# Kernel optimization log

Hardware: AMD Instinct MI355X
Metric: run time of the kernel (lower is better)

Reference implementation:

```python
import math
import jax, jax.numpy as jnp
import numpy as np

B, L, D, H = 8, 4096, 512, 8
FACTOR = 1


def setup_inputs() -> dict:
    key = jax.random.key(0)
    ks = jax.random.split(key, 8)
    scale = 0.02
    return {
        "queries": jax.random.normal(ks[0], (B, L, D), dtype=jnp.float32),
        "keys": jax.random.normal(ks[1], (B, L, D), dtype=jnp.float32),
        "values": jax.random.normal(ks[2], (B, L, D), dtype=jnp.float32),
        "Wq": jax.random.normal(ks[3], (D, D), dtype=jnp.float32) * scale,
        "bq": jnp.zeros((D,), dtype=jnp.float32),
        "Wk": jax.random.normal(ks[4], (D, D), dtype=jnp.float32) * scale,
        "bk": jnp.zeros((D,), dtype=jnp.float32),
        "Wv": jax.random.normal(ks[5], (D, D), dtype=jnp.float32) * scale,
        "bv": jnp.zeros((D,), dtype=jnp.float32),
        "Wo": jax.random.normal(ks[6], (D, D), dtype=jnp.float32) * scale,
        "bo": jnp.zeros((D,), dtype=jnp.float32),
    }


def reference(queries, keys, values, Wq, bq, Wk, bk, Wv, bv, Wo, bo):
    b, l, d = queries.shape
    h = H
    e = d // h
    # Projections (torch Linear math; weight stored as [in, out] here)
    q = (queries @ Wq + bq).reshape(b, l, h, e)
    k = (keys @ Wk + bk).reshape(b, l, h, e)
    v = (values @ Wv + bv).reshape(b, l, h, e)
    # [B, H, E, L]
    qp = q.transpose(0, 2, 3, 1)
    kp = k.transpose(0, 2, 3, 1)
    vp = v.transpose(0, 2, 3, 1)
    # FFT cross-correlation over the time axis
    qf = jnp.fft.rfft(qp, axis=-1)
    kf = jnp.fft.rfft(kp, axis=-1)
    corr = jnp.fft.irfft(qf * jnp.conj(kf), n=l, axis=-1)  # [B,H,E,L]
    # time_delay_agg_training
    top_k = int(FACTOR * math.log(l))
    mean_value = corr.mean(axis=(1, 2))  # [B, L] (mean over head then channel)
    _, index = jax.lax.top_k(mean_value.mean(axis=0), top_k)  # [K] shared delays
    weights = mean_value[:, index]  # [B, K]
    tmp_corr = jax.nn.softmax(weights, axis=-1)  # [B, K]
    # roll(values, -delay) along time == gather at (t + delay) mod L
    idx = (jnp.arange(l)[None, :] + index[:, None]) % l  # [K, L]
    gathered = jnp.take(vp, idx, axis=-1)  # [B, H, E, K, L]
    agg = jnp.einsum("bhekl,bk->bhel", gathered, tmp_corr)  # weighted MAC over delays
    out = agg.transpose(0, 3, 1, 2).reshape(b, l, h * e)  # [B, L, D]
    return out @ Wo + bo
```

## Files before the change

kernel.cpp:

```cpp
#include <hip/hip_runtime.h>
#include <math.h>

#define LSEQ 4096
#define DMODEL 512
#define BB 8
#define TOPK 8
#define ML (BB * LSEQ)
#define FFT_CH 2
#define NGRP (DMODEL / FFT_CH)
#define PPH 2052

typedef unsigned short u16;
typedef unsigned int u32;
typedef float f32x4 __attribute__((ext_vector_type(4)));
typedef short s16x8 __attribute__((ext_vector_type(8)));
typedef u16 u16x8 __attribute__((ext_vector_type(8)));

__device__ __forceinline__ u16 rne_bf16(float f) {
    u32 u = __float_as_uint(f);
    return (u16)((u + 0x7FFF + ((u >> 16) & 1)) >> 16);
}

__device__ __forceinline__ uint4 cvt8(const float4 f0, const float4 f1) {
    float fs[8] = {f0.x, f0.y, f0.z, f0.w, f1.x, f1.y, f1.z, f1.w};
    u32 h[4];
#pragma unroll
    for (int p = 0; p < 4; ++p) {
        u32 u0 = __float_as_uint(fs[2 * p]);
        u32 u1 = __float_as_uint(fs[2 * p + 1]);
        u32 h0 = u0 + 0x7FFF + ((u0 >> 16) & 1);
        u32 h1 = u1 + 0x7FFF + ((u1 >> 16) & 1);
        h[p] = __builtin_amdgcn_perm(h1, h0, 0x07060302u);
    }
    return make_uint4(h[0], h[1], h[2], h[3]);
}

#if defined(__has_builtin)
#if __has_builtin(__builtin_amdgcn_global_load_lds)
#define HAVE_GLL 1
#endif
#endif

__device__ __forceinline__ void gload_lds16(const u16* g, u16* lbase, int lane) {
#ifdef HAVE_GLL
    __builtin_amdgcn_global_load_lds((const __attribute__((address_space(1))) void*)g,
                                     (__attribute__((address_space(3))) void*)lbase, 16, 0, 0);
#else
    *(uint4*)(lbase + lane * 8) = *(const uint4*)g;
#endif
}

__device__ __forceinline__ void fft16(float (&zr)[16], float (&zi)[16]) {
    const float C1 = 0.92387953251128674f, S1 = 0.38268343236508978f, R2 = 0.70710678118654752f;
#define BF0(i, j) { float ar=zr[i],ai=zi[i],br=zr[j],bi=zi[j]; zr[i]=ar+br; zi[i]=ai+bi; zr[j]=ar-br; zi[j]=ai-bi; }
#define BFW(i, j, wr, wi) { float ar=zr[i],ai=zi[i],br=zr[j],bi=zi[j]; zr[i]=ar+br; zi[i]=ai+bi; float dr=ar-br, di=ai-bi; zr[j]=dr*(wr)-di*(wi); zi[j]=dr*(wi)+di*(wr); }
#define BFI(i, j) { float ar=zr[i],ai=zi[i],br=zr[j],bi=zi[j]; zr[i]=ar+br; zi[i]=ai+bi; float dr=ar-br, di=ai-bi; zr[j]=di; zi[j]=-dr; }
    BF0(0, 8); BFW(1, 9, C1, -S1); BFW(2, 10, R2, -R2); BFW(3, 11, S1, -C1);
    BFI(4, 12); BFW(5, 13, -S1, -C1); BFW(6, 14, -R2, -R2); BFW(7, 15, -C1, -S1);
    BF0(0, 4); BFW(1, 5, R2, -R2); BFI(2, 6); BFW(3, 7, -R2, -R2);
    BF0(8, 12); BFW(9, 13, R2, -R2); BFI(10, 14); BFW(11, 15, -R2, -R2);
    BF0(0, 2); BFI(1, 3); BF0(4, 6); BFI(5, 7);
    BF0(8, 10); BFI(9, 11); BF0(12, 14); BFI(13, 15);
    BF0(0, 1); BF0(2, 3); BF0(4, 5); BF0(6, 7);
    BF0(8, 9); BF0(10, 11); BF0(12, 13); BF0(14, 15);
#undef BF0
#undef BFW
#undef BFI
}

template <bool WRITEBACK>
__device__ __forceinline__ void fft4096_r16_core(float* __restrict__ lre, float* __restrict__ lim, int t,
                                                 float (&ozr)[16], float (&ozi)[16]) {
    constexpr int REV16[16] = {0, 8, 4, 12, 2, 10, 6, 14, 1, 9, 5, 13, 3, 11, 7, 15};
    float zr[16], zi[16];
#pragma unroll
    for (int gg = 0; gg < 16; ++gg) {
        int n = 256 * gg + t;
        int p = n ^ ((gg & 3) << 2) ^ ((gg & 1) << 4);
        zr[gg] = lre[p]; zi[gg] = lim[p];
    }
    fft16(zr, zi);
    {
        const int n1 = t >> 4;
        float w1i, w1r;
        __sincosf(-0.0245436926061702596f * (float)n1, &w1i, &w1r);
        float wr = 1.f, wi = 0.f;
#pragma unroll
        for (int k0 = 0; k0 < 16; ++k0) {
            float vr = zr[REV16[k0]], vi = zi[REV16[k0]];
            if (k0) {
                float nr = wr * w1r - wi * w1i;
                wi = wr * w1i + wi * w1r;
                wr = nr;
                float tr = vr * wr - vi * wi;
                vi = vr * wi + vi * wr;
                vr = tr;
            }
            int n = 256 * k0 + t;
            int p = n ^ ((k0 & 3) << 2) ^ ((k0 & 1) << 4);
            lre[p] = vr; lim[p] = vi;
        }
    }
    __syncthreads();
    {
        const int k0 = t >> 4, n2 = t & 15;
        const int x0 = ((k0 & 3) << 2) | ((k0 & 1) << 4);
#pragma unroll
        for (int gg = 0; gg < 16; ++gg) {
            int n = 256 * k0 + 16 * gg + n2;
            zr[gg] = lre[n ^ x0]; zi[gg] = lim[n ^ x0];
        }
        fft16(zr, zi);
        float wbi, wbr, wsi, wsr;
        __sincosf(-0.00153398078788564123f * (float)(n2 * k0), &wbi, &wbr);
        __sincosf(-0.0245436926061702596f * (float)n2, &wsi, &wsr);
        float wr = wbr, wi = wbi;
#pragma unroll
        for (int k1 = 0; k1 < 16; ++k1) {
            float vr = zr[REV16[k1]], vi = zi[REV16[k1]];
            if (k1) {
                float nr = wr * wsr - wi * wsi;
                wi = wr * wsi + wi * wsr;
                wr = nr;
            }
            float tr = vr * wr - vi * wi;
            vi = vr * wi + vi * wr;
            vr = tr;
            int n = 256 * k0 + 16 * k1 + n2;
            lre[n ^ x0] = vr; lim[n ^ x0] = vi;
        }
    }
    __syncthreads();
    {
        const int k0 = t & 15, k1 = t >> 4;
        const int nb4 = 64 * k0 + 4 * k1;
        const int xv = (k0 & 3) | ((k0 & 1) << 2);
#pragma unroll
        for (int i = 0; i < 4; ++i) {
            int p4 = (nb4 + i) ^ xv;
            float4 fr = *(const float4*)&lre[4 * p4];
            float4 fi = *(const float4*)&lim[4 * p4];
            ozr[4 * i + 0] = fr.x; ozr[4 * i + 1] = fr.y; ozr[4 * i + 2] = fr.z; ozr[4 * i + 3] = fr.w;
            ozi[4 * i + 0] = fi.x; ozi[4 * i + 1] = fi.y; ozi[4 * i + 2] = fi.z; ozi[4 * i + 3] = fi.w;
        }
        fft16(ozr, ozi);
        if constexpr (WRITEBACK) {
            __syncthreads();
#pragma unroll
            for (int r = 0; r < 16; ++r) {
                const int k2 = REV16[r];
                lre[t + 256 * k2] = ozr[r];
                lim[t + 256 * k2] = ozi[r];
            }
            __syncthreads();
        }
    }
}

__global__ __launch_bounds__(256) void fft_cross(const u16* __restrict__ Qtb,
                                                 const u16* __restrict__ Ktb,
                                                 float* __restrict__ Ppart) {
    __shared__ float lre[4096];
    __shared__ float lim[4096];
    constexpr int REV16[16] = {0, 8, 4, 12, 2, 10, 6, 14, 1, 9, 5, 13, 3, 11, 7, 15};
    const int t = threadIdx.x;
    const int b = blockIdx.x / NGRP;
    const int g = blockIdx.x % NGRP;

    float2 acc[8];
#pragma unroll
    for (int i = 0; i < 8; ++i) acc[i] = make_float2(0.f, 0.f);
    float accn = 0.f;

    const uint4* q8 = (const uint4*)(Qtb + (size_t)(g * FFT_CH) * ML + (size_t)b * LSEQ);
    const uint4* k8 = (const uint4*)(Ktb + (size_t)(g * FFT_CH) * ML + (size_t)b * LSEQ);

    uint4 pq[2], pk[2];
    pq[0] = q8[t]; pq[1] = q8[t + 256];
    pk[0] = k8[t]; pk[1] = k8[t + 256];

    for (int c = 0; c < FFT_CH; ++c) {
        __syncthreads();
#pragma unroll
        for (int i = 0; i < 2; ++i) {
            const int u = t + 256 * i;
            const uint4 vq = pq[i], vk = pk[i];
#pragma unroll
            for (int hh = 0; hh < 2; ++hh) {
                const int v = 2 * u + hh;
                const int key = (v >> 6) & 15;
                const int p4 = v ^ (key & 3) ^ ((key & 1) << 2);
                const u32 w0 = hh ? vq.z : vq.x;
                const u32 w1 = hh ? vq.w : vq.y;
                float4 fa = make_float4(__uint_as_float(w0 << 16), __uint_as_float(w0 & 0xFFFF0000u),
                                        __uint_as_float(w1 << 16), __uint_as_float(w1 & 0xFFFF0000u));
                *(float4*)&lre[4 * p4] = fa;
                const u32 x0 = hh ? vk.z : vk.x;
                const u32 x1 = hh ? vk.w : vk.y;
                float4 fb = make_float4(__uint_as_float(x0 << 16), __uint_as_float(x0 & 0xFFFF0000u),
                                        __uint_as_float(x1 << 16), __uint_as_float(x1 & 0xFFFF0000u));
                *(float4*)&lim[4 * p4] = fb;
            }
        }
        if (c + 1 < FFT_CH) {
            const uint4* qn = q8 + (size_t)(c + 1) * (ML / 8);
            const uint4* kn = k8 + (size_t)(c + 1) * (ML / 8);
            pq[0] = qn[t]; pq[1] = qn[t + 256];
            pk[0] = kn[t]; pk[1] = kn[t + 256];
        }
        __syncthreads();
        float ozr[16], ozi[16];
        fft4096_r16_core<true>(lre, lim, t, ozr, ozi);
#pragma unroll
        for (int i = 0; i < 8; ++i) {
            const int j = i * 256 + t;
            const int nj = (4096 - j) & 4095;
            const int r = REV16[i];
            float zfr = ozr[r], zfi = ozi[r];
            float znr = lre[nj], zni = lim[nj];
            float qr = 0.5f * (zfr + znr);
            float qi = 0.5f * (zfi - zni);
            float kr = 0.5f * (zfi + zni);
            float ki = -0.5f * (zfr - znr);
            acc[i].x += qr * kr + qi * ki;
            acc[i].y += qi * kr - qr * ki;
        }
        if (t == 0) accn += ozr[1] * ozi[1];
    }
    float2* Pp = (float2*)Ppart + (size_t)blockIdx.x * PPH;
#pragma unroll
    for (int i = 0; i < 8; ++i) Pp[i * 256 + t] = acc[i];
    if (t == 0) Pp[2048] = make_float2(accn, 0.f);
}

template <bool TOUT, bool BIAS>
__device__ __forceinline__ void gemm_bf16_body(const u16* __restrict__ A,
                                               const u16* __restrict__ B,
                                               const float* __restrict__ bias,
                                               u16* __restrict__ Cv, int lin, int tid,
                                               u16* sA, u16* sB) {
    const int t = (lin & 7) * 128 + (lin >> 3);
    const int bm = (t >> 2) * 128;
    const int bn = (t & 3) * 128;
    const int lane = tid & 63, wid = tid >> 6;
    const int wm = wid >> 1, wn = wid & 1;
    const int l15 = lane & 15, kg = lane >> 4;

    const int srow = lane >> 3, sc = lane & 7;

    f32x4 acc[4][4] = {};

    for (int k0 = 0; k0 < 512; k0 += 64) {
        __syncthreads();
#pragma unroll
        for (int i = 0; i < 4; ++i) {
            const int grp = wid * 4 + i;
            const int row = 8 * grp + srow;
            gload_lds16(A + (size_t)(bm + row) * 512 + k0 + ((sc ^ (row & 7)) << 3),
                        sA + grp * 512, lane);
        }
#pragma unroll
        for (int i = 0; i < 4; ++i) {
            const int grp = wid * 4 + i;
            const int row = 8 * grp + srow;
            gload_lds16(B + (size_t)(bn + row) * 512 + k0 + ((sc ^ (row & 7)) << 3),
                        sB + grp * 512, lane);
        }
        __syncthreads();
#pragma unroll
        for (int kk = 0; kk < 2; ++kk) {
            const int cb = kk * 4 + kg;
            s16x8 af[4], bf[4];
#pragma unroll
            for (int mi = 0; mi < 4; ++mi) {
                const int row = wm * 64 + mi * 16 + l15;
                af[mi] = *(const s16x8*)&sA[row * 64 + (((cb ^ (row & 7))) << 3)];
            }
#pragma unroll
            for (int ni = 0; ni < 4; ++ni) {
                const int row = wn * 64 + ni * 16 + l15;
                bf[ni] = *(const s16x8*)&sB[row * 64 + (((cb ^ (row & 7))) << 3)];
            }
#pragma unroll
            for (int ni = 0; ni < 4; ++ni)
#pragma unroll
                for (int mi = 0; mi < 4; ++mi)
                    acc[mi][ni] = __builtin_amdgcn_mfma_f32_16x16x32_bf16(af[mi], bf[ni], acc[mi][ni], 0, 0, 0);
        }
    }
    if constexpr (TOUT) {
#pragma unroll
        for (int ni = 0; ni < 4; ++ni) {
            const int d = bn + wn * 64 + ni * 16 + l15;
#pragma unroll
            for (int mi = 0; mi < 4; ++mi) {
                const int rb = bm + wm * 64 + mi * 16 + (kg << 2);
                ushort4 o;
                o.x = rne_bf16(acc[mi][ni][0]); o.y = rne_bf16(acc[mi][ni][1]);
                o.z = rne_bf16(acc[mi][ni][2]); o.w = rne_bf16(acc[mi][ni][3]);
                *(ushort4*)&Cv[(size_t)d * ML + rb] = o;
            }
        }
    } else {
#pragma unroll
        for (int ni = 0; ni < 4; ++ni) {
            const int col = bn + wn * 64 + ni * 16 + l15;
            const float bvv = BIAS ? bias[col] : 0.0f;
#pragma unroll
            for (int mi = 0; mi < 4; ++mi) {
                const int rb = bm + wm * 64 + mi * 16 + (kg << 2);
#pragma unroll
                for (int r = 0; r < 4; ++r)
                    Cv[(size_t)(rb + r) * 512 + col] = rne_bf16(acc[mi][ni][r] + bvv);
            }
        }
    }
}

__global__ __launch_bounds__(256) void gemm2(const u16* __restrict__ Qb,
                                             const u16* __restrict__ Mh, u16* __restrict__ Qtb,
                                             const u16* __restrict__ Vb,
                                             const u16* __restrict__ Wch, const float* __restrict__ bc,
                                             u16* __restrict__ VOb) {
    __shared__ __align__(16) u16 smem[16384];
    const int g = blockIdx.x;
    const int q = g >> 1, r = g & 1;
    if (r == 0)
        gemm_bf16_body<true, false>(Qb, Mh, nullptr, Qtb, q, threadIdx.x, smem, smem + 8192);
    else
        gemm_bf16_body<false, true>(Vb, Wch, bc, VOb, q, threadIdx.x, smem, smem + 8192);
}

__global__ __launch_bounds__(256) void prep_stream(const float* __restrict__ Wq, const float* __restrict__ Wk,
                                                   const float* __restrict__ Wv, const float* __restrict__ Wo,
                                                   const float* __restrict__ bvec, const float* __restrict__ bo,
                                                   u16* __restrict__ Mh, u16* __restrict__ Wch,
                                                   float* __restrict__ bc,
                                                   const float* __restrict__ keys, u16* __restrict__ Ktb,
                                                   const float* __restrict__ queries, u16* __restrict__ Qb,
                                                   const float* __restrict__ values, u16* __restrict__ Vb) {
    __shared__ __align__(16) char smem[16896];
    const int bx = blockIdx.x;
    const int tid = threadIdx.x;
    if (bx < 128) {
        float (*As)[64] = (float (*)[64])smem;
        float (*Ws)[64] = (float (*)[64])(smem + 4096);
        const bool isM = bx < 64;
        const int id = bx & 63;
        const int bm = (id >> 3) * 64, bn = (id & 7) * 64;
        const int tx = tid & 15, ty = tid >> 4;
        float acc[4][4] = {};
        const int arow = tid >> 2, ak4 = tid & 3;
        const int wrow = tid >> 4, wc4 = tid & 15;
        const float* Abase = isM ? Wq : Wv;
        for (int k0 = 0; k0 < 512; k0 += 16) {
            float4 av = *(const float4*)&Abase[(size_t)(bm + arow) * 512 + k0 + ak4 * 4];
            float4 wv4;
            if (isM) wv4 = *(const float4*)&Wk[(size_t)(bn + arow) * 512 + k0 + ak4 * 4];
            else     wv4 = *(const float4*)&Wo[(size_t)(k0 + wrow) * 512 + bn + wc4 * 4];
            __syncthreads();
            As[ak4 * 4 + 0][arow] = av.x;
            As[ak4 * 4 + 1][arow] = av.y;
            As[ak4 * 4 + 2][arow] = av.z;
            As[ak4 * 4 + 3][arow] = av.w;
            if (isM) {
                Ws[ak4 * 4 + 0][arow] = wv4.x;
                Ws[ak4 * 4 + 1][arow] = wv4.y;
                Ws[ak4 * 4 + 2][arow] = wv4.z;
                Ws[ak4 * 4 + 3][arow] = wv4.w;
            } else {
                *(float4*)&Ws[wrow][wc4 * 4] = wv4;
            }
            __syncthreads();
#pragma unroll
            for (int k = 0; k < 16; ++k) {
                float4 a = *(const float4*)&As[k][ty * 4];
                float4 b = *(const float4*)&Ws[k][tx * 4];
                acc[0][0] += a.x * b.x; acc[0][1] += a.x * b.y; acc[0][2] += a.x * b.z; acc[0][3] += a.x * b.w;
                acc[1][0] += a.y * b.x; acc[1][1] += a.y * b.y; acc[1][2] += a.y * b.z; acc[1][3] += a.y * b.w;
                acc[2][0] += a.z * b.x; acc[2][1] += a.z * b.y; acc[2][2] += a.z * b.z; acc[2][3] += a.z * b.w;
                acc[3][0] += a.w * b.x; acc[3][1] += a.w * b.y; acc[3][2] += a.w * b.z; acc[3][3] += a.w * b.w;
            }
        }
        u16* dh = isM ? Mh : Wch;
#pragma unroll
        for (int i = 0; i < 4; ++i)
#pragma unroll
            for (int j = 0; j < 4; ++j) {
                const int a = bm + ty * 4 + i;
                const int n = bn + tx * 4 + j;
                dh[(size_t)n * 512 + a] = rne_bf16(acc[i][j]);
            }
    } else if (bx < 144) {
        float (*red)[32] = (float (*)[32])smem;
        const int n0 = (bx - 128) * 32;
        const int nl = tid & 31, jg = tid >> 5;
        float partial = 0.f;
        for (int s = 0; s < 64; ++s) {
            int j = jg + 8 * s;
            partial += bvec[j] * Wo[(size_t)j * 512 + n0 + nl];
        }
        red[jg][nl] = partial;
        __syncthreads();
        if (tid < 32) {
            float s2 = 0.f;
            for (int r2 = 0; r2 < 8; ++r2) s2 += red[r2][tid];
            bc[n0 + tid] = s2 + bo[n0 + tid];
        }
    } else if (bx < 144 + 4096) {
        float* Ts = (float*)smem;
        const int tb = bx - 144;
        const int bd = (tb & 7) * 64;
        const int bm = (tb >> 3) * 64;
        const int rr = tid >> 2, c4 = tid & 3;
#pragma unroll
        for (int i = 0; i < 4; ++i) {
            const int c0 = (c4 + 4 * i) * 4;
            float4 v = *(const float4*)&keys[(size_t)(bm + rr) * DMODEL + bd + c0];
            Ts[rr * 65 + c0 + 0] = v.x; Ts[rr * 65 + c0 + 1] = v.y;
            Ts[rr * 65 + c0 + 2] = v.z; Ts[rr * 65 + c0 + 3] = v.w;
        }
        __syncthreads();
        const int dl = tid >> 2, m4 = tid & 3;
#pragma unroll
        for (int i = 0; i < 4; ++i) {
            const int m0 = (m4 + 4 * i) * 4;
            ushort4 o;
            o.x = rne_bf16(Ts[(m0 + 0) * 65 + dl]);
            o.y = rne_bf16(Ts[(m0 + 1) * 65 + dl]);
            o.z = rne_bf16(Ts[(m0 + 2) * 65 + dl]);
            o.w = rne_bf16(Ts[(m0 + 3) * 65 + dl]);
            *(ushort4*)&Ktb[(size_t)(bd + dl) * ML + bm + m0] = o;
        }
    } else {
        const int idx = bx - (144 + 4096);
        const float* src = (idx < 8192) ? queries : values;
        u16* dst = (idx < 8192) ? Qb : Vb;
        const size_t base = (size_t)(idx & 8191) * 2048 + tid * 8;
        float4 f0 = *(const float4*)&src[base];
        float4 f1 = *(const float4*)&src[base + 4];
        *(uint4*)&dst[base] = cvt8(f0, f1);
    }
}

__global__ __launch_bounds__(256) void reduce_ppart(const float2* __restrict__ Pp,
                                                    float2* __restrict__ Pred4) {
    const int j = blockIdx.x * 256 + threadIdx.x;
    const int b = blockIdx.y;
    const int z = blockIdx.z;
    if (j > 2048) return;
    float sr = 0.f, si = 0.f;
    const float2* base = Pp + (size_t)b * NGRP * PPH + j;
    for (int g = z * 64; g < z * 64 + 64; ++g) {
        float2 p = base[(size_t)g * PPH];
        sr += p.x;
        si += p.y;
    }
    Pred4[((size_t)z * BB + b) * PPH + j] = make_float2(sr, si);
}

__global__ __launch_bounds__(256) void ifft_mean(const float2* __restrict__ Pred4,
                                                 float* __restrict__ mv) {
    __shared__ float lre[4096];
    __shared__ float lim[4096];
    constexpr int REV16[16] = {0, 8, 4, 12, 2, 10, 6, 14, 1, 9, 5, 13, 3, 11, 7, 15};
    const int t = threadIdx.x;
    const int b = blockIdx.x;
    for (int j = t; j < 4096; j += 256) {
        const int jj = (j <= 2048) ? j : 4096 - j;
        float sr = 0.f, si = 0.f;
#pragma unroll
        for (int z = 0; z < 4; ++z) {
            float2 p = Pred4[((size_t)z * BB + b) * PPH + jj];
            sr += p.x;
            si += p.y;
        }
        if (j > 2048) si = -si;
        int key = (j >> 8) & 15;
        int ph = j ^ ((key & 3) << 2) ^ ((key & 1) << 4);
        lre[ph] = sr;
        lim[ph] = -si;
    }
    __syncthreads();
    float ozr[16], ozi[16];
    fft4096_r16_core<false>(lre, lim, t, ozr, ozi);
    const float scale = 1.0f / (4096.0f * 512.0f);
#pragma unroll
    for (int i = 0; i < 16; ++i)
        mv[(size_t)b * 4096 + t + 256 * i] = ozr[REV16[i]] * scale;
}

__global__ __launch_bounds__(1024) void topk_softmax(const float* __restrict__ mv,
                                                     int* __restrict__ idxO,
                                                     float* __restrict__ tcO) {
    __shared__ float vals[4096];
    __shared__ float wv[16];
    __shared__ int wix[16];
    __shared__ int sidx[TOPK];
    const int tid = threadIdx.x;
    const int lane = tid & 63, wvid = tid >> 6;
    for (int j = tid; j < 4096; j += 1024) {
        float s = 0.f;
        for (int b = 0; b < BB; ++b) s += mv[(size_t)b * 4096 + j];
        vals[j] = s * 0.125f;
    }
    __syncthreads();
    for (int k = 0; k < TOPK; ++k) {
        float best = -INFINITY;
        int bi = 0x7fffffff;
        for (int j = tid; j < 4096; j += 1024) {
            float v = vals[j];
            if (v > best) { best = v; bi = j; }
        }
#pragma unroll
        for (int off = 32; off > 0; off >>= 1) {
            float ov = __shfl_down(best, off);
            int oi = __shfl_down(bi, off);
            if (ov > best || (ov == best && oi < bi)) { best = ov; bi = oi; }
        }
        if (lane == 0) { wv[wvid] = best; wix[wvid] = bi; }
        __syncthreads();
        if (wvid == 0) {
            best = (lane < 16) ? wv[lane] : -INFINITY;
            bi = (lane < 16) ? wix[lane] : 0x7fffffff;
#pragma unroll
            for (int off = 8; off > 0; off >>= 1) {
                float ov = __shfl_down(best, off);
                int oi = __shfl_down(bi, off);
                if (ov > best || (ov == best && oi < bi)) { best = ov; bi = oi; }
            }
            if (lane == 0) {
                sidx[k] = bi;
                idxO[k] = bi;
                vals[bi] = -INFINITY;
            }
        }
        __syncthreads();
    }
    if (tid < BB) {
        float w[TOPK];
        float m = -INFINITY;
        for (int k = 0; k < TOPK; ++k) {
            w[k] = mv[(size_t)tid * 4096 + sidx[k]];
            m = fmaxf(m, w[k]);
        }
        float s = 0.f;
        for (int k = 0; k < TOPK; ++k) { w[k] = expf(w[k] - m); s += w[k]; }
        float inv = 1.0f / s;
        for (int k = 0; k < TOPK; ++k) tcO[tid * TOPK + k] = w[k] * inv;
    }
}

__global__ __launch_bounds__(256) void gather_out(const u16* __restrict__ VO,
                                                  const int* __restrict__ idx,
                                                  const float* __restrict__ tc,
                                                  float* __restrict__ out) {
    const int e = blockIdx.x * 256 + threadIdx.x;
    const int d8 = e & 63;
    const int l = (e >> 6) & 4095;
    const int b = e >> 18;
    float s[8] = {};
#pragma unroll
    for (int k = 0; k < TOPK; ++k) {
        const int src = (l + idx[k]) & 4095;
        const float w = tc[b * TOPK + k];
        uint4 v = *(const uint4*)&VO[((size_t)(b * 4096 + src)) * 512 + d8 * 8];
        s[0] += w * __uint_as_float(v.x << 16);
        s[1] += w * __uint_as_float(v.x & 0xFFFF0000u);
        s[2] += w * __uint_as_float(v.y << 16);
        s[3] += w * __uint_as_float(v.y & 0xFFFF0000u);
        s[4] += w * __uint_as_float(v.z << 16);
        s[5] += w * __uint_as_float(v.z & 0xFFFF0000u);
        s[6] += w * __uint_as_float(v.w << 16);
        s[7] += w * __uint_as_float(v.w & 0xFFFF0000u);
    }
    const size_t ob = ((size_t)(b * 4096 + l)) * 512 + d8 * 8;
    *(float4*)&out[ob]     = make_float4(s[0], s[1], s[2], s[3]);
    *(float4*)&out[ob + 4] = make_float4(s[4], s[5], s[6], s[7]);
}

extern "C" void kernel_launch(void* const* d_in, const int* in_sizes, int n_in,
                              void* d_out, int out_size, void* d_ws, size_t ws_size,
                              hipStream_t stream) {
    const float* queries = (const float*)d_in[0];
    const float* keys    = (const float*)d_in[1];
    const float* values  = (const float*)d_in[2];
    const float* Wq = (const float*)d_in[3];
    const float* Wk = (const float*)d_in[5];
    const float* Wv = (const float*)d_in[7];
    const float* bv = (const float*)d_in[8];
    const float* Wo = (const float*)d_in[9];
    const float* bo = (const float*)d_in[10];
    float* out = (float*)d_out;

    const size_t SZ = (size_t)ML * DMODEL;
    u16* Qb  = (u16*)d_ws;
    u16* Vb  = Qb + SZ;
    u16* Qtb = Vb + SZ;
    u16* Ktb = Qtb + SZ;
    u16* VOb = Ktb + SZ;
    float* Pp    = (float*)(VOb + SZ);
    float* Pred4 = Pp + (size_t)BB * NGRP * PPH * 2;
    float* mv    = Pred4 + (size_t)4 * BB * PPH * 2;
    int*   idx   = (int*)(mv + 32768);
    float* tc    = mv + 32768 + 16;
    float* bc    = mv + 32768 + 96;
    u16* Mh  = (u16*)(bc + 512);
    u16* Wch = Mh + 262144;

    dim3 blk(256);

    prep_stream<<<dim3(144 + 4096 + 16384), blk, 0, stream>>>(
        Wq, Wk, Wv, Wo, bv, bo, Mh, Wch, bc, keys, Ktb, queries, Qb, values, Vb);

    gemm2<<<dim3(2048), blk, 0, stream>>>(Qb, Mh, Qtb, Vb, Wch, bc, VOb);

    fft_cross<<<dim3(BB * NGRP), blk, 0, stream>>>(Qtb, Ktb, Pp);

    reduce_ppart<<<dim3(9, BB, 4), blk, 0, stream>>>((const float2*)Pp, (float2*)Pred4);

    ifft_mean<<<dim3(BB), blk, 0, stream>>>((const float2*)Pred4, mv);

    topk_softmax<<<dim3(1), dim3(1024), 0, stream>>>(mv, idx, tc);

    gather_out<<<dim3((BB * LSEQ * (DMODEL / 8)) / 256), blk, 0, stream>>>(VOb, idx, tc, out);
}
```

Measured before the change: 222.9 us.

## Rebalance kernel phases to overlap values conversion and V GEMM with FFT

The three launches are reorganised into phases. Phase1 converts only queries and keys. Phase2 interleaves the Q GEMM with the values fp32-to-bf16 conversion. Phase3 interleaves the FFT cross-correlation blocks with the V·Wo GEMM, so compute-bound and memory-bound blocks share the GPU at the same time. The FFT writeback also stores only the odd radix outputs, and the j=0 mirror read now uses registers instead of shared memory, which trims LDS traffic. The risks are a larger shared-memory footprint per phase3 block and uneven block durations within a launch.

```diff
diff --git a/kernel.cpp b/kernel.cpp
--- a/kernel.cpp
+++ b/kernel.cpp
@@ -147,7 +147,7 @@
         if constexpr (WRITEBACK) {
             __syncthreads();
 #pragma unroll
-            for (int r = 0; r < 16; ++r) {
+            for (int r = 1; r < 16; r += 2) {
                 const int k2 = REV16[r];
                 lre[t + 256 * k2] = ozr[r];
                 lim[t + 256 * k2] = ozi[r];
@@ -157,15 +157,14 @@
     }
 }
 
-__global__ __launch_bounds__(256) void fft_cross(const u16* __restrict__ Qtb,
-                                                 const u16* __restrict__ Ktb,
-                                                 float* __restrict__ Ppart) {
-    __shared__ float lre[4096];
-    __shared__ float lim[4096];
+__device__ __forceinline__ void fft_cross_body(const u16* __restrict__ Qtb,
+                                               const u16* __restrict__ Ktb,
+                                               float* __restrict__ Ppart,
+                                               int fb, int t,
+                                               float* __restrict__ lre, float* __restrict__ lim) {
     constexpr int REV16[16] = {0, 8, 4, 12, 2, 10, 6, 14, 1, 9, 5, 13, 3, 11, 7, 15};
-    const int t = threadIdx.x;
-    const int b = blockIdx.x / NGRP;
-    const int g = blockIdx.x % NGRP;
+    const int b = fb / NGRP;
+    const int g = fb % NGRP;
 
     float2 acc[8];
 #pragma unroll
@@ -197,9 +196,9 @@
                 *(float4*)&lre[4 * p4] = fa;
                 const u32 x0 = hh ? vk.z : vk.x;
                 const u32 x1 = hh ? vk.w : vk.y;
-                float4 fb = make_float4(__uint_as_float(x0 << 16), __uint_as_float(x0 & 0xFFFF0000u),
-                                        __uint_as_float(x1 << 16), __uint_as_float(x1 & 0xFFFF0000u));
-                *(float4*)&lim[4 * p4] = fb;
+                float4 fb4 = make_float4(__uint_as_float(x0 << 16), __uint_as_float(x0 & 0xFFFF0000u),
+                                         __uint_as_float(x1 << 16), __uint_as_float(x1 & 0xFFFF0000u));
+                *(float4*)&lim[4 * p4] = fb4;
             }
         }
         if (c + 1 < FFT_CH) {
@@ -217,7 +216,9 @@
             const int nj = (4096 - j) & 4095;
             const int r = REV16[i];
             float zfr = ozr[r], zfi = ozi[r];
-            float znr = lre[nj], zni = lim[nj];
+            float znr, zni;
+            if (j) { znr = lre[nj]; zni = lim[nj]; }
+            else   { znr = zfr;     zni = zfi;     }
             float qr = 0.5f * (zfr + znr);
             float qi = 0.5f * (zfi - zni);
             float kr = 0.5f * (zfi + zni);
@@ -227,7 +228,7 @@
         }
         if (t == 0) accn += ozr[1] * ozi[1];
     }
-    float2* Pp = (float2*)Ppart + (size_t)blockIdx.x * PPH;
+    float2* Pp = (float2*)Ppart + (size_t)fb * PPH;
 #pragma unroll
     for (int i = 0; i < 8; ++i) Pp[i * 256 + t] = acc[i];
     if (t == 0) Pp[2048] = make_float2(accn, 0.f);
@@ -317,28 +318,13 @@
     }
 }
 
-__global__ __launch_bounds__(256) void gemm2(const u16* __restrict__ Qb,
-                                             const u16* __restrict__ Mh, u16* __restrict__ Qtb,
-                                             const u16* __restrict__ Vb,
-                                             const u16* __restrict__ Wch, const float* __restrict__ bc,
-                                             u16* __restrict__ VOb) {
-    __shared__ __align__(16) u16 smem[16384];
-    const int g = blockIdx.x;
-    const int q = g >> 1, r = g & 1;
-    if (r == 0)
-        gemm_bf16_body<true, false>(Qb, Mh, nullptr, Qtb, q, threadIdx.x, smem, smem + 8192);
-    else
-        gemm_bf16_body<false, true>(Vb, Wch, bc, VOb, q, threadIdx.x, smem, smem + 8192);
-}
-
-__global__ __launch_bounds__(256) void prep_stream(const float* __restrict__ Wq, const float* __restrict__ Wk,
-                                                   const float* __restrict__ Wv, const float* __restrict__ Wo,
-                                                   const float* __restrict__ bvec, const float* __restrict__ bo,
-                                                   u16* __restrict__ Mh, u16* __restrict__ Wch,
-                                                   float* __restrict__ bc,
-                                                   const float* __restrict__ keys, u16* __restrict__ Ktb,
-                                                   const float* __restrict__ queries, u16* __restrict__ Qb,
-                                                   const float* __restrict__ values, u16* __restrict__ Vb) {
+__global__ __launch_bounds__(256) void phase1(const float* __restrict__ Wq, const float* __restrict__ Wk,
+                                              const float* __restrict__ Wv, const float* __restrict__ Wo,
+                                              const float* __restrict__ bvec, const float* __restrict__ bo,
+                                              u16* __restrict__ Mh, u16* __restrict__ Wch,
+                                              float* __restrict__ bc,
+                                              const float* __restrict__ keys, u16* __restrict__ Ktb,
+                                              const float* __restrict__ queries, u16* __restrict__ Qb) {
     __shared__ __align__(16) char smem[16896];
     const int bx = blockIdx.x;
     const int tid = threadIdx.x;
@@ -434,12 +420,53 @@
         }
     } else {
         const int idx = bx - (144 + 4096);
-        const float* src = (idx < 8192) ? queries : values;
-        u16* dst = (idx < 8192) ? Qb : Vb;
-        const size_t base = (size_t)(idx & 8191) * 2048 + tid * 8;
-        float4 f0 = *(const float4*)&src[base];
-        float4 f1 = *(const float4*)&src[base + 4];
-        *(uint4*)&dst[base] = cvt8(f0, f1);
+        const size_t base0 = (size_t)idx * 8192 + tid * 8;
+#pragma unroll
+        for (int it = 0; it < 4; ++it) {
+            const size_t base = base0 + it * 2048;
+            float4 f0 = *(const float4*)&queries[base];
+            float4 f1 = *(const float4*)&queries[base + 4];
+            *(uint4*)&Qb[base] = cvt8(f0, f1);
+        }
+    }
+}
+
+__global__ __launch_bounds__(256) void phase2(const u16* __restrict__ Qb,
+                                              const u16* __restrict__ Mh, u16* __restrict__ Qtb,
+                                              const float* __restrict__ values, u16* __restrict__ Vb) {
+    __shared__ __align__(16) u16 smem[16384];
+    const int g = blockIdx.x;
+    const int q = g / 3, r = g % 3;
+    const int tid = threadIdx.x;
+    if (r == 0) {
+        gemm_bf16_body<true, false>(Qb, Mh, nullptr, Qtb, q, tid, smem, smem + 8192);
+    } else {
+        const int idx = q * 2 + (r - 1);
+        const size_t base0 = (size_t)idx * 8192 + tid * 8;
+#pragma unroll
+        for (int it = 0; it < 4; ++it) {
+            const size_t base = base0 + it * 2048;
+            float4 f0 = *(const float4*)&values[base];
+            float4 f1 = *(const float4*)&values[base + 4];
+            *(uint4*)&Vb[base] = cvt8(f0, f1);
+        }
+    }
+}
+
+__global__ __launch_bounds__(256) void phase3(const u16* __restrict__ Qtb,
+                                              const u16* __restrict__ Ktb,
+                                              float* __restrict__ Pp,
+                                              const u16* __restrict__ Vb,
+                                              const u16* __restrict__ Wch, const float* __restrict__ bc,
+                                              u16* __restrict__ VOb) {
+    __shared__ __align__(16) char smem[32768];
+    const int g = blockIdx.x;
+    const int q = g / 3, r = g % 3;
+    const int tid = threadIdx.x;
+    if (r < 2) {
+        fft_cross_body(Qtb, Ktb, Pp, q * 2 + r, tid, (float*)smem, (float*)(smem + 16384));
+    } else {
+        gemm_bf16_body<false, true>(Vb, Wch, bc, VOb, q, tid, (u16*)smem, (u16*)smem + 8192);
     }
 }
 
@@ -610,12 +637,12 @@
 
     dim3 blk(256);
 
-    prep_stream<<<dim3(144 + 4096 + 16384), blk, 0, stream>>>(
-        Wq, Wk, Wv, Wo, bv, bo, Mh, Wch, bc, keys, Ktb, queries, Qb, values, Vb);
-
-    gemm2<<<dim3(2048), blk, 0, stream>>>(Qb, Mh, Qtb, Vb, Wch, bc, VOb);
-
-    fft_cross<<<dim3(BB * NGRP), blk, 0, stream>>>(Qtb, Ktb, Pp);
+    phase1<<<dim3(144 + 4096 + 2048), blk, 0, stream>>>(
+        Wq, Wk, Wv, Wo, bv, bo, Mh, Wch, bc, keys, Ktb, queries, Qb);
+
+    phase2<<<dim3(3072), blk, 0, stream>>>(Qb, Mh, Qtb, values, Vb);
+
+    phase3<<<dim3(3072), blk, 0, stream>>>(Qtb, Ktb, Pp, Vb, Wch, bc, VOb);
 
     reduce_ppart<<<dim3(9, BB, 4), blk, 0, stream>>>((const float2*)Pp, (float2*)Pred4);
 
```

After: 246.4 us. +10.5%, slower.
